# Performance work log

Measured on AMD Instinct MI355X. Metric: run time of the kernel, lower is better.

## Reference

```python
import jax, jax.numpy as jnp
import numpy as np

LP, LQ, B, D, H = 500, 64, 64, 256, 150  # lp, lq, batch_size, in_size, hidden_size*2


def setup_inputs() -> dict:
    key = jax.random.key(0)
    ks = jax.random.split(key, 12)
    s = 0.05
    f32 = jnp.float32
    return {
        "Up": jax.random.normal(ks[0], (LP, B, D), f32),
        "Uq": jax.random.normal(ks[1], (LQ, B, D), f32),
        "Wp": jax.random.normal(ks[2], (H, 2 * D), f32) * s,
        "Wq": jax.random.normal(ks[3], (H, 2 * D), f32) * s,
        "Wv": jax.random.normal(ks[4], (H, H), f32) * s,
        "Wg": jax.random.normal(ks[5], (4 * D, 4 * D), f32) * s,
        "V": jax.random.normal(ks[6], (B, H), f32),        # per-batch attention vector (squeezed [B,H,1])
        "v0": jax.random.normal(ks[7], (B, H), f32),       # initial GRU state self.v
        "W_ih": jax.random.normal(ks[8], (3 * H, 2 * D), f32) * s,
        "W_hh": jax.random.normal(ks[9], (3 * H, H), f32) * s,
        "b_ih": jax.random.normal(ks[10], (3 * H,), f32) * s,
        "b_hh": jax.random.normal(ks[11], (3 * H,), f32) * s,
    }


def reference(Up, Uq, Wp, Wq, Wv, Wg, V, v0, W_ih, W_hh, b_ih, b_hh):
    Din = Up.shape[2]
    # torch.cat([U, U[arange]], dim=2) == duplicate features
    Up2 = jnp.concatenate([Up, Up], axis=2)  # [lp, B, 2D]
    Uq2 = jnp.concatenate([Uq, Uq], axis=2)  # [lq, B, 2D]
    # Wq(Uq2) is loop-invariant in the original loop; hoist it (same math)
    Wuq = jnp.einsum('qbd,hd->qbh', Uq2, Wq)  # [lq, B, H]

    def gru_cell(x, h):
        gi = x @ W_ih.T + b_ih  # [B, 3H]
        gh = h @ W_hh.T + b_hh
        i_r, i_z, i_n = jnp.split(gi, 3, axis=1)
        h_r, h_z, h_n = jnp.split(gh, 3, axis=1)
        r = jax.nn.sigmoid(i_r + h_r)
        z = jax.nn.sigmoid(i_z + h_z)
        n = jnp.tanh(i_n + r * h_n)
        return (1.0 - z) * n + z * h

    def step(v, up_i):  # up_i: [B, 2D], v: [B, H]
        Wup = up_i @ Wp.T                                   # [B, H]
        x = jnp.tanh(Wup[None] + Wuq + (v @ Wv.T)[None])    # [lq, B, H]
        s = jnp.einsum('qbh,bh->bq', x, V)                  # bmm(x^T, V).squeeze
        a = jax.nn.softmax(s, axis=1)                       # [B, lq]
        c = jnp.einsum('bq,qbd->bd', a, Uq2)                # [B, 2D]
        r = jnp.concatenate([up_i, c], axis=1)              # [B, 4D]
        g = jax.nn.sigmoid(r @ Wg.T)
        r = g * r
        c_ = r[:, 2 * Din:]                                 # gated context -> GRU input
        v_new = gru_cell(c_, v)
        return v_new, v_new

    _, vs = jax.lax.scan(step, v0, Up2)  # [lp, B, H]
    # dropout is identity in eval mode
    return vs
```

## Files before the change

### kernel.cpp

```cpp
#include <hip/hip_runtime.h>
#include <hip/hip_fp16.h>

#define LP 500

typedef _Float16 h2f __attribute__((ext_vector_type(2)));
typedef _Float16 h8f __attribute__((ext_vector_type(8)));

constexpr size_t OFF_WVH2 = 0;
constexpr size_t OFF_WGF2 = 46208;
constexpr size_t OFF_WIH2 = 111744;
constexpr size_t OFF_WPF  = 227456;
constexpr size_t OFF_WQF  = 265856;
constexpr size_t OFF_WUQ  = 304256;
constexpr size_t OFF_P1   = 918656;
constexpr size_t OFF_WG1  = OFF_P1;
constexpr size_t OFF_GUH  = 5718656;
constexpr size_t OFF_UPT  = 13910656;
constexpr size_t OFF_UQT  = 22102656;
constexpr size_t OFF_UQT2 = OFF_UQT;
constexpr size_t WS_FLOATS = 23151232;

__device__ __forceinline__ float fast_rcp(float x) { return __builtin_amdgcn_rcpf(x); }
__device__ __forceinline__ float sigm(float x)   { return fast_rcp(1.f + __expf(-x)); }
__device__ __forceinline__ float tanh_f(float x) { return 1.f - 2.f * fast_rcp(1.f + __expf(2.f * x)); }

__global__ __launch_bounds__(256) void k_prep(const float* __restrict__ Wp, const float* __restrict__ Wq,
                                              const float* __restrict__ Wg, const float* __restrict__ Wv,
                                              const float* __restrict__ Whh, const float* __restrict__ Wih,
                                              float* __restrict__ ws) {
    int i = blockIdx.x * 256 + threadIdx.x;
    if (i < 46208) {
        int k2 = i / 608, m = i - k2 * 608;
        float lo = 0.f, hi = 0.f;
        if (k2 < 75 && m < 600) {
            if (m < 150) { lo = Wv[m * 150 + 2 * k2]; hi = Wv[m * 150 + 2 * k2 + 1]; }
            else { int mm = m - 150; lo = Whh[mm * 150 + 2 * k2]; hi = Whh[mm * 150 + 2 * k2 + 1]; }
        }
        ((h2f*)(ws + OFF_WVH2))[i] = h2f{(_Float16)lo, (_Float16)hi};
        return;
    }
    i -= 46208;
    if (i < 65536) {
        int k2 = i >> 9, j = i & 511;
        int d = 2 * k2;
        size_t r = (size_t)(512 + j) * 1024;
        float lo = Wg[r + 512 + d] + Wg[r + 768 + d];
        float hi = Wg[r + 512 + d + 1] + Wg[r + 768 + d + 1];
        ((h2f*)(ws + OFF_WGF2))[i] = h2f{(_Float16)lo, (_Float16)hi};
        return;
    }
    i -= 65536;
    if (i < 115712) {
        int k2 = i / 452, m = i - k2 * 452;
        float lo = 0.f, hi = 0.f;
        if (m < 450) { lo = Wih[m * 512 + 2 * k2]; hi = Wih[m * 512 + 2 * k2 + 1]; }
        ((h2f*)(ws + OFF_WIH2))[i] = h2f{(_Float16)lo, (_Float16)hi};
        return;
    }
    i -= 115712;
    if (i < 38400) { int h = i >> 8, d = i & 255; ws[OFF_WPF + i] = Wp[h * 512 + d] + Wp[h * 512 + 256 + d]; return; }
    i -= 38400;
    if (i < 38400) { int h = i >> 8, d = i & 255; ws[OFF_WQF + i] = Wq[h * 512 + d] + Wq[h * 512 + 256 + d]; return; }
    i -= 38400;
    if (i < 131072) { int j = i >> 8, d = i & 255; size_t r = (size_t)(512 + j) * 1024; ws[OFF_WG1 + i] = Wg[r + d] + Wg[r + 256 + d]; return; }
}

__global__ __launch_bounds__(256) void k_tr(const float* __restrict__ X, float* __restrict__ XT) {
    __shared__ float tile[64][65];
    size_t base = (size_t)blockIdx.x * 16384;
    for (int ph = 0; ph < 4; ++ph) {
        for (int i = threadIdx.x; i < 4096; i += 256) {
            int b = i >> 6, dl = i & 63;
            tile[b][dl] = X[base + (size_t)b * 256 + ph * 64 + dl];
        }
        __syncthreads();
        for (int i = threadIdx.x; i < 4096; i += 256) {
            int d = i >> 6, bl = i & 63;
            XT[base + (size_t)(ph * 64 + d) * 64 + bl] = tile[bl][d];
        }
        __syncthreads();
    }
}

__global__ __launch_bounds__(256) void k_gemm(const float* __restrict__ XT, const float* __restrict__ Wf,
                                              float* __restrict__ outF, _Float16* __restrict__ outH,
                                              int Hrows, int tilesPerT) {
    __shared__ float OL[64 * 33];
    int bidx = blockIdx.x;
    int t = bidx / tilesPerT, tile = bidx - t * tilesPerT;
    int w = threadIdx.x >> 6, lane = threadIdx.x & 63;
    int h0 = __builtin_amdgcn_readfirstlane(tile * 32 + w * 8);
    const float* x = XT + (size_t)t * 16384;
    float acc[8];
    const float* wr[8];
#pragma unroll
    for (int r = 0; r < 8; ++r) {
        int hr = h0 + r; if (hr >= Hrows) hr = Hrows - 1;
        wr[r] = Wf + (size_t)hr * 256;
        acc[r] = 0.f;
    }
    for (int d = 0; d < 256; d += 4) {
        float cv0 = x[(d + 0) * 64 + lane];
        float cv1 = x[(d + 1) * 64 + lane];
        float cv2 = x[(d + 2) * 64 + lane];
        float cv3 = x[(d + 3) * 64 + lane];
#pragma unroll
        for (int r = 0; r < 8; ++r) {
            float4 wv = *(const float4*)(wr[r] + d);
            acc[r] += cv0 * wv.x + cv1 * wv.y + cv2 * wv.z + cv3 * wv.w;
        }
    }
#pragma unroll
    for (int r = 0; r < 8; ++r) { int hl = w * 8 + r; OL[lane * 33 + hl] = acc[r]; }
    __syncthreads();
    int hbase = tile * 32;
    int nh = Hrows - hbase; if (nh > 32) nh = 32;
    for (int i = threadIdx.x; i < 64 * nh; i += 256) {
        int b = i / nh, hl = i - b * nh;
        float val = OL[b * 33 + hl];
        size_t idx = (size_t)t * 64 * Hrows + (size_t)b * Hrows + hbase + hl;
        if (outF) outF[idx] = val;
        else outH[idx] = (_Float16)val;
    }
}

__global__ __launch_bounds__(256) void k_uqt(const float* __restrict__ Uq, h2f* __restrict__ UqT2) {
    int b = blockIdx.x, d = threadIdx.x;
    for (int q2 = 0; q2 < 32; ++q2) {
        float lo = Uq[(size_t)(2 * q2) * 16384 + b * 256 + d];
        float hi = Uq[(size_t)(2 * q2 + 1) * 16384 + b * 256 + d];
        UqT2[(size_t)b * 8192 + q2 * 256 + d] = h2f{(_Float16)lo, (_Float16)hi};
    }
}

__global__ __launch_bounds__(512, 2) void k_scan8(
    const float* __restrict__ V, const float* __restrict__ v0,
    const float* __restrict__ bih, const float* __restrict__ bhh,
    const float* __restrict__ ws, float* __restrict__ out) {
    __shared__ __attribute__((aligned(16))) float red[2048];
    __shared__ __attribute__((aligned(16))) _Float16 vh[152];
    __shared__ float pbf[152];
    __shared__ float ghf[452];
    __shared__ float Vb[152];
    __shared__ float bihL[452];
    __shared__ float bhhL[452];
    __shared__ float vf[152];
    __shared__ float sa[64];
    __shared__ __attribute__((aligned(8))) h2f sah[32];
    __shared__ float ccf[256];
    __shared__ __attribute__((aligned(8))) h2f cchp[128];
    __shared__ __attribute__((aligned(8))) h2f c_p[256];
    __shared__ float gif[452];
    __shared__ __attribute__((aligned(16))) h2f uql[8192];
    __shared__ __attribute__((aligned(16))) h2f wihl[60 * 452];

    const int tid = threadIdx.x, b = blockIdx.x;
    const int lane = tid & 63;
    const h2f* Wvh2 = (const h2f*)(ws + OFF_WVH2);
    const h2f* Wih2 = (const h2f*)(ws + OFF_WIH2);
    const h2f* UqT2b = (const h2f*)(ws + OFF_UQT2) + (size_t)b * 8192;
    const float* WuqG = ws + OFF_WUQ;
    const float* P1 = ws + OFF_P1;
    const _Float16* GuH = (const _Float16*)(ws + OFF_GUH);

    const int p1_ks = tid / 152, p1_mq = tid - p1_ks * 152;
    const h2f* wv_base = Wvh2 + (size_t)(p1_ks * 25) * 608 + 4 * p1_mq;
    const int p2_qs = tid >> 6, p2_mq = tid & 63;
    const h2f* uq_base = uql + (size_t)(p2_qs * 4) * 256 + 4 * p2_mq;
    const int p3_ks = tid >> 7, p3_mq = tid & 127;
    const int p4_ks = tid / 113, p4_mq = tid - p4_ks * 113;
    const h2f* wih_base = Wih2 + (size_t)(p4_ks * 64) * 452 + 4 * p4_mq;

    const h2f* Wgf2 = (const h2f*)(ws + OFF_WGF2);
    h8f wgr[32];
#pragma unroll
    for (int i = 0; i < 32; ++i)
        wgr[i] = *(const h8f*)(Wgf2 + (size_t)(p3_ks * 32 + i) * 512 + 4 * p3_mq);

    const int w8 = tid >> 6;
    _Float16 wq[24];
#pragma unroll
    for (int i = 0; i < 8; ++i)
#pragma unroll
        for (int it = 0; it < 3; ++it) {
            int idx = lane + 64 * it;
            wq[i * 3 + it] = (_Float16)(idx < 150 ? WuqG[(size_t)(w8 * 8 + i) * 9600 + b * 150 + idx] : 0.f);
        }

    {
        const h8f* s = (const h8f*)UqT2b;
        h8f* dstu = (h8f*)uql;
        for (int u = tid; u < 2048; u += 512) dstu[u] = s[u];
        h8f* dstw = (h8f*)wihl;
        for (int u = tid; u < 6780; u += 512) {
            int slot = u / 113, off = u - slot * 113;
            int ks = slot / 15, i = slot - ks * 15;
            dstw[u] = *(const h8f*)(Wih2 + (size_t)(ks * 64 + i) * 452 + off * 4);
        }
    }

    for (int i = tid; i < 150; i += 512) { Vb[i] = V[b * 150 + i]; float v = v0[b * 150 + i]; vf[i] = v; vh[i] = (_Float16)v; }
    for (int i = tid; i < 450; i += 512) { bihL[i] = bih[i]; bhhL[i] = bhh[i]; }
    if (tid < 2) vh[150 + tid] = (_Float16)0.f;
    __syncthreads();

    for (int t = 0; t < LP; ++t) {
        float p1v = 0.f;
        if (tid < 150) p1v = P1[(size_t)t * 9600 + b * 150 + tid];
        float guv = (float)GuH[(size_t)t * 32768 + b * 512 + tid];

        if (tid < 456) {
            const h2f* vh2 = (const h2f*)vh;
            float a0 = 0.f, a1 = 0.f, a2 = 0.f, a3 = 0.f;
#pragma unroll 5
            for (int i = 0; i < 25; ++i) {
                h8f w = *(const h8f*)(wv_base + (size_t)i * 608);
                h2f x = vh2[p1_ks * 25 + i];
                a0 = __builtin_amdgcn_fdot2(h2f{w[0], w[1]}, x, a0, false);
                a1 = __builtin_amdgcn_fdot2(h2f{w[2], w[3]}, x, a1, false);
                a2 = __builtin_amdgcn_fdot2(h2f{w[4], w[5]}, x, a2, false);
                a3 = __builtin_amdgcn_fdot2(h2f{w[6], w[7]}, x, a3, false);
            }
            *(float4*)(red + p1_ks * 608 + 4 * p1_mq) = float4{a0, a1, a2, a3};
        }
        __syncthreads();
        for (int m = tid; m < 600; m += 512) {
            float s = red[m] + red[608 + m] + red[1216 + m];
            if (m < 150) pbf[m] = s + p1v;
            else ghf[m - 150] = s + bhhL[m - 150];
        }
        __syncthreads();
        {
#pragma unroll
            for (int i = 0; i < 8; ++i) {
                int q = w8 * 8 + i;
                float part = 0.f;
#pragma unroll
                for (int it = 0; it < 3; ++it) {
                    int idx = lane + 64 * it;
                    if (idx < 150)
                        part += tanh_f(pbf[idx] + (float)wq[i * 3 + it]) * Vb[idx];
                }
                part += __shfl_xor(part, 32); part += __shfl_xor(part, 16);
                part += __shfl_xor(part, 8);  part += __shfl_xor(part, 4);
                part += __shfl_xor(part, 2);  part += __shfl_xor(part, 1);
                if (lane == 0) sa[q] = part;
            }
        }
        __syncthreads();
        if (tid < 64) {
            float s = sa[tid];
            float m = s;
            m = fmaxf(m, __shfl_xor(m, 32)); m = fmaxf(m, __shfl_xor(m, 16));
            m = fmaxf(m, __shfl_xor(m, 8));  m = fmaxf(m, __shfl_xor(m, 4));
            m = fmaxf(m, __shfl_xor(m, 2));  m = fmaxf(m, __shfl_xor(m, 1));
            float e = __expf(s - m);
            float su = e;
            su += __shfl_xor(su, 32); su += __shfl_xor(su, 16); su += __shfl_xor(su, 8);
            su += __shfl_xor(su, 4);  su += __shfl_xor(su, 2);  su += __shfl_xor(su, 1);
            float a = e * fast_rcp(su);
            float an = __shfl_xor(a, 1);
            if ((tid & 1) == 0) sah[tid >> 1] = h2f{(_Float16)a, (_Float16)an};
        }
        __syncthreads();
        {
            float a0 = 0.f, a1 = 0.f, a2 = 0.f, a3 = 0.f;
#pragma unroll
            for (int i = 0; i < 4; ++i) {
                h8f u = *(const h8f*)(uq_base + (size_t)i * 256);
                h2f ap = sah[p2_qs * 4 + i];
                a0 = __builtin_amdgcn_fdot2(h2f{u[0], u[1]}, ap, a0, false);
                a1 = __builtin_amdgcn_fdot2(h2f{u[2], u[3]}, ap, a1, false);
                a2 = __builtin_amdgcn_fdot2(h2f{u[4], u[5]}, ap, a2, false);
                a3 = __builtin_amdgcn_fdot2(h2f{u[6], u[7]}, ap, a3, false);
            }
            *(float4*)(red + p2_qs * 256 + 4 * p2_mq) = float4{a0, a1, a2, a3};
        }
        __syncthreads();
        if (tid < 256) {
            float cc = 0.f;
#pragma unroll
            for (int s8 = 0; s8 < 8; ++s8) cc += red[s8 * 256 + tid];
            ccf[tid] = cc;
            float cn = __shfl_xor(cc, 1);
            if ((tid & 1) == 0) cchp[tid >> 1] = h2f{(_Float16)cc, (_Float16)cn};
        }
        __syncthreads();
        {
            float a0 = 0.f, a1 = 0.f, a2 = 0.f, a3 = 0.f;
#pragma unroll
            for (int i = 0; i < 32; ++i) {
                h2f cp = cchp[p3_ks * 32 + i];
                h8f w = wgr[i];
                a0 = __builtin_amdgcn_fdot2(h2f{w[0], w[1]}, cp, a0, false);
                a1 = __builtin_amdgcn_fdot2(h2f{w[2], w[3]}, cp, a1, false);
                a2 = __builtin_amdgcn_fdot2(h2f{w[4], w[5]}, cp, a2, false);
                a3 = __builtin_amdgcn_fdot2(h2f{w[6], w[7]}, cp, a3, false);
            }
            *(float4*)(red + p3_ks * 512 + 4 * p3_mq) = float4{a0, a1, a2, a3};
        }
        __syncthreads();
        {
            float s = guv;
#pragma unroll
            for (int s4 = 0; s4 < 4; ++s4) s += red[s4 * 512 + tid];
            float val = sigm(s) * ccf[tid & 255];
            float vn2 = __shfl_xor(val, 1);
            if ((tid & 1) == 0) c_p[tid >> 1] = h2f{(_Float16)val, (_Float16)vn2};
        }
        __syncthreads();
        if (tid < 452) {
            float a0 = 0.f, a1 = 0.f, a2 = 0.f, a3 = 0.f;
#pragma unroll
            for (int i = 0; i < 15; ++i) {
                h8f w = *(const h8f*)(wihl + (size_t)(p4_ks * 15 + i) * 452 + 4 * p4_mq);
                h2f cp = c_p[p4_ks * 64 + i];
                a0 = __builtin_amdgcn_fdot2(h2f{w[0], w[1]}, cp, a0, false);
                a1 = __builtin_amdgcn_fdot2(h2f{w[2], w[3]}, cp, a1, false);
                a2 = __builtin_amdgcn_fdot2(h2f{w[4], w[5]}, cp, a2, false);
                a3 = __builtin_amdgcn_fdot2(h2f{w[6], w[7]}, cp, a3, false);
            }
#pragma unroll 16
            for (int i = 15; i < 64; ++i) {
                h8f w = *(const h8f*)(wih_base + (size_t)i * 452);
                h2f cp = c_p[p4_ks * 64 + i];
                a0 = __builtin_amdgcn_fdot2(h2f{w[0], w[1]}, cp, a0, false);
                a1 = __builtin_amdgcn_fdot2(h2f{w[2], w[3]}, cp, a1, false);
                a2 = __builtin_amdgcn_fdot2(h2f{w[4], w[5]}, cp, a2, false);
                a3 = __builtin_amdgcn_fdot2(h2f{w[6], w[7]}, cp, a3, false);
            }
            *(float4*)(red + p4_ks * 456 + 4 * p4_mq) = float4{a0, a1, a2, a3};
        }
        __syncthreads();
        if (tid < 450) {
            gif[tid] = red[tid] + red[456 + tid] + red[912 + tid] + red[1368 + tid];
        }
        __syncthreads();
        if (tid < 150) {
            float r = sigm(gif[tid] + bihL[tid] + ghf[tid]);
            float z = sigm(gif[150 + tid] + bihL[150 + tid] + ghf[150 + tid]);
            float n = tanh_f(gif[300 + tid] + bihL[300 + tid] + r * ghf[300 + tid]);
            float vn = (1.f - z) * n + z * vf[tid];
            vf[tid] = vn;
            vh[tid] = (_Float16)vn;
            out[(size_t)t * 9600 + b * 150 + tid] = vn;
        }
        __syncthreads();
    }
}

extern "C" void kernel_launch(void* const* d_in, const int* in_sizes, int n_in,
                              void* d_out, int out_size, void* d_ws, size_t ws_size,
                              hipStream_t stream) {
    const float* Up  = (const float*)d_in[0];
    const float* Uq  = (const float*)d_in[1];
    const float* Wp  = (const float*)d_in[2];
    const float* Wq  = (const float*)d_in[3];
    const float* Wv  = (const float*)d_in[4];
    const float* Wg  = (const float*)d_in[5];
    const float* V   = (const float*)d_in[6];
    const float* v0  = (const float*)d_in[7];
    const float* Wih = (const float*)d_in[8];
    const float* Whh = (const float*)d_in[9];
    const float* bih = (const float*)d_in[10];
    const float* bhh = (const float*)d_in[11];
    float* out = (float*)d_out;
    float* ws = (float*)d_ws;

    if (ws_size < WS_FLOATS * sizeof(float)) return;

    k_prep<<<1701, 256, 0, stream>>>(Wp, Wq, Wg, Wv, Whh, Wih, ws);
    k_tr<<<500, 256, 0, stream>>>(Up, ws + OFF_UPT);
    k_tr<<<64, 256, 0, stream>>>(Uq, ws + OFF_UQT);
    k_gemm<<<8000, 256, 0, stream>>>(ws + OFF_UPT, ws + OFF_WG1, nullptr, (_Float16*)(ws + OFF_GUH), 512, 16);
    k_gemm<<<2500, 256, 0, stream>>>(ws + OFF_UPT, ws + OFF_WPF, ws + OFF_P1, nullptr, 150, 5);
    k_gemm<<<320, 256, 0, stream>>>(ws + OFF_UQT, ws + OFF_WQF, ws + OFF_WUQ, nullptr, 150, 5);
    k_uqt<<<64, 256, 0, stream>>>(Uq, (h2f*)(ws + OFF_UQT2));
    k_scan8<<<64, 512, 0, stream>>>(V, v0, bih, bhh, ws, out);
}
```

Baseline: 6.523 ms.

## Widen recurrent scan block to 768 threads with finer K-splits

Grows the per-batch scan block from 512 to 768 threads. Each matvec stage (Wv, Wg, W_ih) and the attention-score loop is re-partitioned so every thread handles a shorter K-slice, and the extra partial sums are reduced from a larger shared buffer. The aim is to shorten the serial per-timestep latency of the 500-step recurrence by spreading work over more waves. In exchange it adds reduction work and fewer registers per thread, since the Wg rows cached in registers shrink to 22. Fewer W_ih rows are now kept in LDS, so more of them are read from global memory each step.

```diff
diff --git a/kernel.cpp b/kernel.cpp
--- a/kernel.cpp
+++ b/kernel.cpp
@@ -133,11 +133,11 @@
     }
 }
 
-__global__ __launch_bounds__(512, 2) void k_scan8(
+__global__ __launch_bounds__(768, 3) void k_scan10(
     const float* __restrict__ V, const float* __restrict__ v0,
     const float* __restrict__ bih, const float* __restrict__ bhh,
     const float* __restrict__ ws, float* __restrict__ out) {
-    __shared__ __attribute__((aligned(16))) float red[2048];
+    __shared__ __attribute__((aligned(16))) float red[3072];
     __shared__ __attribute__((aligned(16))) _Float16 vh[152];
     __shared__ float pbf[152];
     __shared__ float ghf[452];
@@ -148,11 +148,11 @@
     __shared__ float sa[64];
     __shared__ __attribute__((aligned(8))) h2f sah[32];
     __shared__ float ccf[256];
-    __shared__ __attribute__((aligned(8))) h2f cchp[128];
+    __shared__ __attribute__((aligned(8))) h2f cchp[132];
     __shared__ __attribute__((aligned(8))) h2f c_p[256];
     __shared__ float gif[452];
     __shared__ __attribute__((aligned(16))) h2f uql[8192];
-    __shared__ __attribute__((aligned(16))) h2f wihl[60 * 452];
+    __shared__ __attribute__((aligned(16))) h2f wihl[54 * 452];
 
     const int tid = threadIdx.x, b = blockIdx.x;
     const int lane = tid & 63;
@@ -164,58 +164,64 @@
     const _Float16* GuH = (const _Float16*)(ws + OFF_GUH);
 
     const int p1_ks = tid / 152, p1_mq = tid - p1_ks * 152;
-    const h2f* wv_base = Wvh2 + (size_t)(p1_ks * 25) * 608 + 4 * p1_mq;
+    const h2f* wv_base = Wvh2 + (size_t)(p1_ks * 15) * 608 + 4 * p1_mq;
     const int p2_qs = tid >> 6, p2_mq = tid & 63;
     const h2f* uq_base = uql + (size_t)(p2_qs * 4) * 256 + 4 * p2_mq;
-    const int p3_ks = tid >> 7, p3_mq = tid & 127;
+    const int p3_ks = tid / 128, p3_mq = tid & 127;
     const int p4_ks = tid / 113, p4_mq = tid - p4_ks * 113;
-    const h2f* wih_base = Wih2 + (size_t)(p4_ks * 64) * 452 + 4 * p4_mq;
+    const h2f* wih_base = Wih2 + (size_t)(p4_ks * 44) * 452 + 4 * p4_mq;
 
     const h2f* Wgf2 = (const h2f*)(ws + OFF_WGF2);
-    h8f wgr[32];
-#pragma unroll
-    for (int i = 0; i < 32; ++i)
-        wgr[i] = *(const h8f*)(Wgf2 + (size_t)(p3_ks * 32 + i) * 512 + 4 * p3_mq);
-
-    const int w8 = tid >> 6;
-    _Float16 wq[24];
-#pragma unroll
-    for (int i = 0; i < 8; ++i)
+    h8f wgr[22];
+#pragma unroll
+    for (int i = 0; i < 22; ++i) {
+        int row = p3_ks * 22 + i;
+        wgr[i] = (row < 128) ? *(const h8f*)(Wgf2 + (size_t)row * 512 + 4 * p3_mq) : h8f{};
+    }
+
+    const int w12 = tid >> 6;
+    const int nq = (w12 < 4) ? 6 : 5;
+    const int q0 = (w12 < 4) ? w12 * 6 : 24 + (w12 - 4) * 5;
+    _Float16 wq[18];
+#pragma unroll
+    for (int i = 0; i < 6; ++i)
 #pragma unroll
         for (int it = 0; it < 3; ++it) {
             int idx = lane + 64 * it;
-            wq[i * 3 + it] = (_Float16)(idx < 150 ? WuqG[(size_t)(w8 * 8 + i) * 9600 + b * 150 + idx] : 0.f);
+            wq[i * 3 + it] = (_Float16)((i < nq && idx < 150) ? WuqG[(size_t)(q0 + i) * 9600 + b * 150 + idx] : 0.f);
         }
 
     {
         const h8f* s = (const h8f*)UqT2b;
         h8f* dstu = (h8f*)uql;
-        for (int u = tid; u < 2048; u += 512) dstu[u] = s[u];
+        for (int u = tid; u < 2048; u += 768) dstu[u] = s[u];
         h8f* dstw = (h8f*)wihl;
-        for (int u = tid; u < 6780; u += 512) {
+        for (int u = tid; u < 6102; u += 768) {
             int slot = u / 113, off = u - slot * 113;
-            int ks = slot / 15, i = slot - ks * 15;
-            dstw[u] = *(const h8f*)(Wih2 + (size_t)(ks * 64 + i) * 452 + off * 4);
-        }
-    }
-
-    for (int i = tid; i < 150; i += 512) { Vb[i] = V[b * 150 + i]; float v = v0[b * 150 + i]; vf[i] = v; vh[i] = (_Float16)v; }
-    for (int i = tid; i < 450; i += 512) { bihL[i] = bih[i]; bhhL[i] = bhh[i]; }
+            int ks = slot / 9, i = slot - ks * 9;
+            dstw[u] = *(const h8f*)(Wih2 + (size_t)(ks * 44 + i) * 452 + off * 4);
+        }
+    }
+
+    for (int i = tid; i < 150; i += 768) { Vb[i] = V[b * 150 + i]; float v = v0[b * 150 + i]; vf[i] = v; vh[i] = (_Float16)v; }
+    for (int i = tid; i < 450; i += 768) { bihL[i] = bih[i]; bhhL[i] = bhh[i]; }
     if (tid < 2) vh[150 + tid] = (_Float16)0.f;
+    if (tid < 4) cchp[128 + tid] = h2f{(_Float16)0.f, (_Float16)0.f};
     __syncthreads();
 
     for (int t = 0; t < LP; ++t) {
         float p1v = 0.f;
         if (tid < 150) p1v = P1[(size_t)t * 9600 + b * 150 + tid];
-        float guv = (float)GuH[(size_t)t * 32768 + b * 512 + tid];
-
-        if (tid < 456) {
+        float guv = 0.f;
+        if (tid < 512) guv = (float)GuH[(size_t)t * 32768 + b * 512 + tid];
+
+        if (tid < 760) {
             const h2f* vh2 = (const h2f*)vh;
             float a0 = 0.f, a1 = 0.f, a2 = 0.f, a3 = 0.f;
 #pragma unroll 5
-            for (int i = 0; i < 25; ++i) {
+            for (int i = 0; i < 15; ++i) {
                 h8f w = *(const h8f*)(wv_base + (size_t)i * 608);
-                h2f x = vh2[p1_ks * 25 + i];
+                h2f x = vh2[p1_ks * 15 + i];
                 a0 = __builtin_amdgcn_fdot2(h2f{w[0], w[1]}, x, a0, false);
                 a1 = __builtin_amdgcn_fdot2(h2f{w[2], w[3]}, x, a1, false);
                 a2 = __builtin_amdgcn_fdot2(h2f{w[4], w[5]}, x, a2, false);
@@ -224,27 +230,28 @@
             *(float4*)(red + p1_ks * 608 + 4 * p1_mq) = float4{a0, a1, a2, a3};
         }
         __syncthreads();
-        for (int m = tid; m < 600; m += 512) {
-            float s = red[m] + red[608 + m] + red[1216 + m];
-            if (m < 150) pbf[m] = s + p1v;
-            else ghf[m - 150] = s + bhhL[m - 150];
+        if (tid < 600) {
+            float s = red[tid] + red[608 + tid] + red[1216 + tid] + red[1824 + tid] + red[2432 + tid];
+            if (tid < 150) pbf[tid] = s + p1v;
+            else ghf[tid - 150] = s + bhhL[tid - 150];
         }
         __syncthreads();
         {
 #pragma unroll
-            for (int i = 0; i < 8; ++i) {
-                int q = w8 * 8 + i;
-                float part = 0.f;
-#pragma unroll
-                for (int it = 0; it < 3; ++it) {
-                    int idx = lane + 64 * it;
-                    if (idx < 150)
-                        part += tanh_f(pbf[idx] + (float)wq[i * 3 + it]) * Vb[idx];
+            for (int i = 0; i < 6; ++i) {
+                if (i < nq) {
+                    float part = 0.f;
+#pragma unroll
+                    for (int it = 0; it < 3; ++it) {
+                        int idx = lane + 64 * it;
+                        if (idx < 150)
+                            part += tanh_f(pbf[idx] + (float)wq[i * 3 + it]) * Vb[idx];
+                    }
+                    part += __shfl_xor(part, 32); part += __shfl_xor(part, 16);
+                    part += __shfl_xor(part, 8);  part += __shfl_xor(part, 4);
+                    part += __shfl_xor(part, 2);  part += __shfl_xor(part, 1);
+                    if (lane == 0) sa[q0 + i] = part;
                 }
-                part += __shfl_xor(part, 32); part += __shfl_xor(part, 16);
-                part += __shfl_xor(part, 8);  part += __shfl_xor(part, 4);
-                part += __shfl_xor(part, 2);  part += __shfl_xor(part, 1);
-                if (lane == 0) sa[q] = part;
             }
         }
         __syncthreads();
@@ -263,7 +270,7 @@
             if ((tid & 1) == 0) sah[tid >> 1] = h2f{(_Float16)a, (_Float16)an};
         }
         __syncthreads();
-        {
+        if (tid < 512) {
             float a0 = 0.f, a1 = 0.f, a2 = 0.f, a3 = 0.f;
 #pragma unroll
             for (int i = 0; i < 4; ++i) {
@@ -289,8 +296,8 @@
         {
             float a0 = 0.f, a1 = 0.f, a2 = 0.f, a3 = 0.f;
 #pragma unroll
-            for (int i = 0; i < 32; ++i) {
-                h2f cp = cchp[p3_ks * 32 + i];
+            for (int i = 0; i < 22; ++i) {
+                h2f cp = cchp[p3_ks * 22 + i];
                 h8f w = wgr[i];
                 a0 = __builtin_amdgcn_fdot2(h2f{w[0], w[1]}, cp, a0, false);
                 a1 = __builtin_amdgcn_fdot2(h2f{w[2], w[3]}, cp, a1, false);
@@ -300,40 +307,44 @@
             *(float4*)(red + p3_ks * 512 + 4 * p3_mq) = float4{a0, a1, a2, a3};
         }
         __syncthreads();
-        {
+        if (tid < 512) {
             float s = guv;
 #pragma unroll
-            for (int s4 = 0; s4 < 4; ++s4) s += red[s4 * 512 + tid];
+            for (int s6 = 0; s6 < 6; ++s6) s += red[s6 * 512 + tid];
             float val = sigm(s) * ccf[tid & 255];
             float vn2 = __shfl_xor(val, 1);
             if ((tid & 1) == 0) c_p[tid >> 1] = h2f{(_Float16)val, (_Float16)vn2};
         }
         __syncthreads();
-        if (tid < 452) {
+        if (tid < 678) {
             float a0 = 0.f, a1 = 0.f, a2 = 0.f, a3 = 0.f;
 #pragma unroll
-            for (int i = 0; i < 15; ++i) {
-                h8f w = *(const h8f*)(wihl + (size_t)(p4_ks * 15 + i) * 452 + 4 * p4_mq);
-                h2f cp = c_p[p4_ks * 64 + i];
+            for (int i = 0; i < 9; ++i) {
+                h8f w = *(const h8f*)(wihl + (size_t)(p4_ks * 9 + i) * 452 + 4 * p4_mq);
+                h2f cp = c_p[p4_ks * 44 + i];
                 a0 = __builtin_amdgcn_fdot2(h2f{w[0], w[1]}, cp, a0, false);
                 a1 = __builtin_amdgcn_fdot2(h2f{w[2], w[3]}, cp, a1, false);
                 a2 = __builtin_amdgcn_fdot2(h2f{w[4], w[5]}, cp, a2, false);
                 a3 = __builtin_amdgcn_fdot2(h2f{w[6], w[7]}, cp, a3, false);
             }
 #pragma unroll 16
-            for (int i = 15; i < 64; ++i) {
-                h8f w = *(const h8f*)(wih_base + (size_t)i * 452);
-                h2f cp = c_p[p4_ks * 64 + i];
-                a0 = __builtin_amdgcn_fdot2(h2f{w[0], w[1]}, cp, a0, false);
-                a1 = __builtin_amdgcn_fdot2(h2f{w[2], w[3]}, cp, a1, false);
-                a2 = __builtin_amdgcn_fdot2(h2f{w[4], w[5]}, cp, a2, false);
-                a3 = __builtin_amdgcn_fdot2(h2f{w[6], w[7]}, cp, a3, false);
+            for (int i = 9; i < 44; ++i) {
+                int row = p4_ks * 44 + i;
+                if (row < 256) {
+                    h8f w = *(const h8f*)(wih_base + (size_t)i * 452);
+                    h2f cp = c_p[row];
+                    a0 = __builtin_amdgcn_fdot2(h2f{w[0], w[1]}, cp, a0, false);
+                    a1 = __builtin_amdgcn_fdot2(h2f{w[2], w[3]}, cp, a1, false);
+                    a2 = __builtin_amdgcn_fdot2(h2f{w[4], w[5]}, cp, a2, false);
+                    a3 = __builtin_amdgcn_fdot2(h2f{w[6], w[7]}, cp, a3, false);
+                }
             }
             *(float4*)(red + p4_ks * 456 + 4 * p4_mq) = float4{a0, a1, a2, a3};
         }
         __syncthreads();
         if (tid < 450) {
-            gif[tid] = red[tid] + red[456 + tid] + red[912 + tid] + red[1368 + tid];
+            gif[tid] = red[tid] + red[456 + tid] + red[912 + tid] + red[1368 + tid]
+                     + red[1824 + tid] + red[2280 + tid];
         }
         __syncthreads();
         if (tid < 150) {
@@ -376,5 +387,5 @@
     k_gemm<<<2500, 256, 0, stream>>>(ws + OFF_UPT, ws + OFF_WPF, ws + OFF_P1, nullptr, 150, 5);
     k_gemm<<<320, 256, 0, stream>>>(ws + OFF_UQT, ws + OFF_WQF, ws + OFF_WUQ, nullptr, 150, 5);
     k_uqt<<<64, 256, 0, stream>>>(Uq, (h2f*)(ws + OFF_UQT2));
-    k_scan8<<<64, 512, 0, stream>>>(V, v0, bih, bhh, ws, out);
-}
+    k_scan10<<<64, 768, 0, stream>>>(V, v0, bih, bhh, ws, out);
+}
```

Result: no change. 6.419 ms (-1.6%).
